# Kernel optimization log

Measured on AMD Instinct MI355X. Metric: run time of the kernel, lower is better.

The kernel has to match this reference:

```python
import jax, jax.numpy as jnp
import numpy as np

N_NODES = 50000
N_EDGES = 800000
IN_DIM = 128
HID = 64
HEADS = 4
EDGE_DIM = 3
NEG_SLOPE = 0.2  # PyG GATv2 default


def setup_inputs() -> dict:
    key = jax.random.key(0)
    ks = jax.random.split(key, 16)
    def glorot(k, shape):
        fan_in = shape[0]
        return (jax.random.normal(k, shape, jnp.float32) / jnp.sqrt(jnp.float32(fan_in)))
    x = jax.random.normal(ks[0], (N_NODES, IN_DIM), jnp.float32)
    edge_attr = jax.random.normal(ks[1], (N_EDGES, EDGE_DIM), jnp.float32)
    edge_index = jax.random.randint(ks[2], (2, N_EDGES), 0, N_NODES, jnp.int32)
    # layer 1: GATv2Conv(IN_DIM -> HID, heads=HEADS, edge_dim=3, concat=True)
    W1l = glorot(ks[3], (IN_DIM, HEADS * HID))
    W1r = glorot(ks[4], (IN_DIM, HEADS * HID))
    W1e = glorot(ks[5], (EDGE_DIM, HEADS * HID))
    att1 = glorot(ks[6], (HEADS, HID))
    b1 = jnp.zeros((HEADS * HID,), jnp.float32)
    # layer 2: GATv2Conv(HEADS*HID -> 1, heads=1, edge_dim=3, concat=False)
    W2l = glorot(ks[7], (HEADS * HID, 1))
    W2r = glorot(ks[8], (HEADS * HID, 1))
    W2e = glorot(ks[9], (EDGE_DIM, 1))
    att2 = glorot(ks[10], (1, 1))
    b2 = jnp.zeros((1,), jnp.float32)
    return {"x": x, "edge_attr": edge_attr, "W1l": W1l, "W1r": W1r, "W1e": W1e,
            "att1": att1, "b1": b1, "W2l": W2l, "W2r": W2r, "W2e": W2e,
            "att2": att2, "b2": b2, "edge_index": edge_index}


def _add_self_loops(edge_index, edge_attr, n_nodes):
    # PyG GATv2Conv add_self_loops=True with fill_value='mean' for edge_attr
    loops = jnp.arange(n_nodes, dtype=edge_index.dtype)
    ei = jnp.concatenate([edge_index, jnp.stack([loops, loops])], axis=1)
    loop_attr = jnp.broadcast_to(edge_attr.mean(axis=0, keepdims=True),
                                 (n_nodes, edge_attr.shape[1]))
    ea = jnp.concatenate([edge_attr, loop_attr], axis=0)
    return ei, ea


def _gatv2(x, edge_index, edge_attr, Wl, Wr, We, att, bias, heads, concat):
    n = x.shape[0]
    c = Wl.shape[1] // heads
    src, dst = edge_index[0], edge_index[1]
    xl = (x @ Wl).reshape(n, heads, c)   # source-side transform
    xr = (x @ Wr).reshape(n, heads, c)   # target-side transform
    ef = (edge_attr @ We).reshape(-1, heads, c)
    m = jax.nn.leaky_relu(xl[src] + xr[dst] + ef, NEG_SLOPE)   # [E,H,C]
    logits = jnp.einsum('ehc,hc->eh', m, att)                  # [E,H]
    mx = jax.ops.segment_max(logits, dst, num_segments=n)      # segment softmax over dst
    a = jnp.exp(logits - mx[dst])
    denom = jax.ops.segment_sum(a, dst, num_segments=n)
    alpha = a / denom[dst]                                     # [E,H]
    out = jax.ops.segment_sum(xl[src] * alpha[:, :, None], dst, num_segments=n)  # [N,H,C]
    out = out.reshape(n, heads * c) if concat else out.mean(axis=1)
    return out + bias


def reference(x, edge_attr, W1l, W1r, W1e, att1, b1, W2l, W2r, W2e, att2, b2, edge_index):
    n = x.shape[0]
    ei, ea = _add_self_loops(edge_index, edge_attr, n)
    h = _gatv2(x, ei, ea, W1l, W1r, W1e, att1, b1, HEADS, True)
    h = jax.nn.elu(h)  # dropout identity in eval mode
    gat_scores = _gatv2(h, ei, ea, W2l, W2r, W2e, att2, b2, 1, False).squeeze(-1)
    portfolio_weights = jax.nn.softmax(gat_scores, axis=0)
    return portfolio_weights, gat_scores
```

## Files before the change

kernel.cpp:

```cpp
#include <hip/hip_runtime.h>
#include <hip/hip_bf16.h>
#include <hip/hip_fp16.h>

typedef __attribute__((ext_vector_type(8))) short short8;
typedef __attribute__((ext_vector_type(4))) float floatx4;
typedef _Float16 h2 __attribute__((ext_vector_type(2)));
typedef _Float16 h4 __attribute__((ext_vector_type(4)));
typedef _Float16 h8 __attribute__((ext_vector_type(8)));
typedef __fp16 fp16x2 __attribute__((ext_vector_type(2)));

#define N_NODESC 50000
#define MPAD     50016
#define N_EDGESC 800000
#define E_TOTC   850000
#define IN_DIMC  128
#define FDIM     256
#define HEADSC   4
#define HIDC     64
#define NEG_SLOPE 0.2f
#define RESCALE_THR 8.0f

#define SCAN_TILE 1024
#define SCAN_NB   ((N_NODESC + SCAN_TILE - 1) / SCAN_TILE)

__device__ __forceinline__ float wave_sum(float v){
  #pragma unroll
  for (int m = 32; m > 0; m >>= 1) v += __shfl_xor(v, m, 64);
  return v;
}
__device__ __forceinline__ float wave_max(float v){
  #pragma unroll
  for (int m = 32; m > 0; m >>= 1) v = fmaxf(v, __shfl_xor(v, m, 64));
  return v;
}
__device__ __forceinline__ float g16_sum(float v){
  #pragma unroll
  for (int m = 8; m > 0; m >>= 1) v += __shfl_xor(v, m, 64);
  return v;
}
__device__ __forceinline__ float g16_max(float v){
  #pragma unroll
  for (int m = 8; m > 0; m >>= 1) v = fmaxf(v, __shfl_xor(v, m, 64));
  return v;
}

__device__ __forceinline__ h2 f2h2(float v){
  return __builtin_bit_cast(h2, __builtin_amdgcn_cvt_pkrtz(v, v));
}
__device__ __forceinline__ float fdot2(h2 a, h2 b, float c){
  return __builtin_amdgcn_fdot2(__builtin_bit_cast(fp16x2, a),
                                __builtin_bit_cast(fp16x2, b), c, false);
}

__global__ __launch_bounds__(256) void k_mean(const float* __restrict__ ea,
                                              float* __restrict__ meanacc){
  float s0 = 0.f, s1 = 0.f, s2 = 0.f;
  for (int i = blockIdx.x * blockDim.x + threadIdx.x; i < N_EDGESC;
       i += gridDim.x * blockDim.x){
    s0 += ea[i*3+0]; s1 += ea[i*3+1]; s2 += ea[i*3+2];
  }
  s0 = wave_sum(s0); s1 = wave_sum(s1); s2 = wave_sum(s2);
  __shared__ float red[3][4];
  int lane = threadIdx.x & 63, w = threadIdx.x >> 6;
  if (lane == 0){ red[0][w] = s0; red[1][w] = s1; red[2][w] = s2; }
  __syncthreads();
  if (threadIdx.x == 0){
    float t0 = 0.f, t1 = 0.f, t2 = 0.f;
    for (int i = 0; i < 4; i++){ t0 += red[0][i]; t1 += red[1][i]; t2 += red[2][i]; }
    atomicAdd(&meanacc[0], t0); atomicAdd(&meanacc[1], t1); atomicAdd(&meanacc[2], t2);
  }
}

__global__ __launch_bounds__(256) void k_count(const int* __restrict__ ei,
                                               int* __restrict__ deg){
  int e = blockIdx.x * blockDim.x + threadIdx.x;
  if (e >= N_EDGESC) return;
  atomicAdd(&deg[ei[N_EDGESC + e]], 1);
}

__global__ __launch_bounds__(256) void k_cvtx(const float* __restrict__ x,
                                              _Float16* __restrict__ xb){
  size_t tid = (size_t)blockIdx.x * 256 + threadIdx.x;
  size_t base = tid * 4;
  const size_t NELEM = (size_t)N_NODESC * IN_DIMC;
  h4 o;
  if (base + 3 < NELEM){
    const float4* xp = (const float4*)(x + base);
    float4 v = *xp;
    o[0] = (_Float16)v.x; o[1] = (_Float16)v.y;
    o[2] = (_Float16)v.z; o[3] = (_Float16)v.w;
  } else {
    #pragma unroll
    for (int f = 0; f < 4; f++){
      size_t i = base + f;
      float v = (i < NELEM) ? x[i] : 0.f;
      o[f] = (_Float16)v;
    }
  }
  *(h4*)(xb + base) = o;
}

__global__ __launch_bounds__(256) void k_cvtw(const float* __restrict__ W1l,
                                              const float* __restrict__ W1r,
                                              _Float16* __restrict__ Bfrag){
  int idx = blockIdx.x * 256 + threadIdx.x;
  int mat = idx >> 15;
  int r   = idx & 32767;
  int k   = r >> 8, n = r & 255;
  float v = mat ? W1r[r] : W1l[r];
  int pos = (mat << 15) + (((k >> 3) << 8) + n) * 8 + (k & 7);
  Bfrag[pos] = (_Float16)v;
}

__global__ __launch_bounds__(256) void k_gemm_mfma(const _Float16* __restrict__ xb,
                                                   const _Float16* __restrict__ Bfrag,
                                                   _Float16* __restrict__ xl,
                                                   _Float16* __restrict__ xr){
  const int mat = blockIdx.y;
  const int r0  = blockIdx.x * 32;
  const int w = threadIdx.x >> 6, lane = threadIdx.x & 63;
  const int quad = lane >> 4, l16 = lane & 15;
  const _Float16* Bm = Bfrag + ((size_t)mat << 15);
  _Float16* C = mat ? xr : xl;

  h8 afr[2][4];
  #pragma unroll
  for (int ms = 0; ms < 2; ms++)
    #pragma unroll
    for (int ks = 0; ks < 4; ks++){
      const _Float16* p = xb + (size_t)(r0 + ms*16 + l16) * IN_DIMC + ks*32 + quad*8;
      afr[ms][ks] = *reinterpret_cast<const h8*>(p);
    }
  const int n0 = w * 64;
  floatx4 acc[2][4];
  #pragma unroll
  for (int ms = 0; ms < 2; ms++)
    #pragma unroll
    for (int ns = 0; ns < 4; ns++){
      floatx4 z = {0.f, 0.f, 0.f, 0.f};
      acc[ms][ns] = z;
    }
  #pragma unroll
  for (int ks = 0; ks < 4; ks++){
    #pragma unroll
    for (int ns = 0; ns < 4; ns++){
      int n = n0 + ns*16 + l16;
      int kblk = ks*4 + quad;
      h8 bfr = *reinterpret_cast<const h8*>(Bm + ((size_t)kblk*256 + n)*8);
      acc[0][ns] = __builtin_amdgcn_mfma_f32_16x16x32_f16(afr[0][ks], bfr, acc[0][ns], 0, 0, 0);
      acc[1][ns] = __builtin_amdgcn_mfma_f32_16x16x32_f16(afr[1][ks], bfr, acc[1][ns], 0, 0, 0);
    }
  }
  #pragma unroll
  for (int ms = 0; ms < 2; ms++)
    #pragma unroll
    for (int ns = 0; ns < 4; ns++){
      int col = n0 + ns*16 + l16;
      #pragma unroll
      for (int rg = 0; rg < 4; rg++){
        int row = r0 + ms*16 + quad*4 + rg;
        C[(size_t)row * FDIM + col] = (_Float16)acc[ms][ns][rg];
      }
    }
}

__global__ __launch_bounds__(256) void k_scan_pa(const int* __restrict__ deg,
                                                 int* __restrict__ pre,
                                                 int* __restrict__ bsum){
  int b = blockIdx.x, t = threadIdx.x;
  int lane = t & 63, w = t >> 6;
  int base = b * SCAN_TILE + t * 4;
  int4 v = {0, 0, 0, 0};
  if (base + 3 < N_NODESC){
    v = *(const int4*)(deg + base);
    v.x += 1; v.y += 1; v.z += 1; v.w += 1;
  } else {
    if (base + 0 < N_NODESC) v.x = deg[base + 0] + 1;
    if (base + 1 < N_NODESC) v.y = deg[base + 1] + 1;
    if (base + 2 < N_NODESC) v.z = deg[base + 2] + 1;
    if (base + 3 < N_NODESC) v.w = deg[base + 3] + 1;
  }
  int s = v.x + v.y + v.z + v.w;
  int inc = s;
  #pragma unroll
  for (int off = 1; off < 64; off <<= 1){
    int u = __shfl_up(inc, off, 64);
    if (lane >= off) inc += u;
  }
  __shared__ int wsum[4];
  if (lane == 63) wsum[w] = inc;
  __syncthreads();
  int wadd = 0;
  #pragma unroll
  for (int i = 0; i < 4; i++) if (i < w) wadd += wsum[i];
  int excl = inc - s + wadd;
  if (base + 3 < N_NODESC){
    int4 o;
    o.x = excl; o.y = o.x + v.x; o.z = o.y + v.y; o.w = o.z + v.z;
    *(int4*)(pre + base) = o;
  } else {
    int run = excl;
    if (base + 0 < N_NODESC){ pre[base + 0] = run; run += v.x; }
    if (base + 1 < N_NODESC){ pre[base + 1] = run; run += v.y; }
    if (base + 2 < N_NODESC){ pre[base + 2] = run; run += v.z; }
    if (base + 3 < N_NODESC){ pre[base + 3] = run; }
  }
  if (t == 255) bsum[b] = wsum[0] + wsum[1] + wsum[2] + wsum[3];
}

__global__ __launch_bounds__(64) void k_scan_pb(const int* __restrict__ bsum,
                                                int* __restrict__ boff,
                                                int* __restrict__ offsets){
  int lane = threadIdx.x;
  int s = (lane < SCAN_NB) ? bsum[lane] : 0;
  int inc = s;
  #pragma unroll
  for (int off = 1; off < 64; off <<= 1){
    int u = __shfl_up(inc, off, 64);
    if (lane >= off) inc += u;
  }
  if (lane < SCAN_NB) boff[lane] = inc - s;
  if (lane == 63) offsets[N_NODESC] = inc;
}

__global__ __launch_bounds__(256) void k_scan_pc(const int* __restrict__ pre,
                                                 const int* __restrict__ boff,
                                                 int* __restrict__ offsets,
                                                 int* __restrict__ cursor){
  int b = blockIdx.x;
  int base = b * SCAN_TILE + threadIdx.x * 4;
  int add = boff[b];
  if (base + 3 < N_NODESC){
    int4 p = *(const int4*)(pre + base);
    p.x += add; p.y += add; p.z += add; p.w += add;
    *(int4*)(offsets + base) = p;
    *(int4*)(cursor + base) = p;
  } else {
    #pragma unroll
    for (int f = 0; f < 4; f++){
      int i = base + f;
      if (i < N_NODESC){ int vv = pre[i] + add; offsets[i] = vv; cursor[i] = vv; }
    }
  }
}

__global__ __launch_bounds__(256) void k_scatter(const int* __restrict__ ei,
                                                 const float* __restrict__ ea,
                                                 const float* __restrict__ meanacc,
                                                 const int* __restrict__ offsets,
                                                 int* __restrict__ cursor,
                                                 float4* __restrict__ rec){
  int e = blockIdx.x * blockDim.x + threadIdx.x;
  if (e >= E_TOTC) return;
  int pos; float4 r;
  if (e < N_EDGESC){
    int src = ei[e], dst = ei[N_EDGESC + e];
    r.x = __int_as_float(src);
    r.y = ea[e*3+0]; r.z = ea[e*3+1]; r.w = ea[e*3+2];
    pos = atomicAdd(&cursor[dst], 1);
  } else {
    int i = e - N_EDGESC;
    const float inv = 1.0f / (float)N_EDGESC;
    r.x = __int_as_float(i);
    r.y = meanacc[0]*inv; r.z = meanacc[1]*inv; r.w = meanacc[2]*inv;
    pos = offsets[i + 1] - 1;
  }
  rec[pos] = r;
}

__global__ __launch_bounds__(256, 4) void k_attn1(const int* __restrict__ offsets,
                                                  const float4* __restrict__ rec,
                                                  const _Float16* __restrict__ xl,
                                                  const _Float16* __restrict__ xr,
                                                  const float* __restrict__ W1e,
                                                  const float* __restrict__ att1,
                                                  const float* __restrict__ b1,
                                                  const float* __restrict__ W2l,
                                                  const float* __restrict__ W2r,
                                                  float* __restrict__ sl,
                                                  float* __restrict__ sr){
  const int t = threadIdx.x, lane = t & 63, w = t >> 6;
  const int n = blockIdx.x * 4 + w;
  const int half = lane >> 5, l32 = lane & 31;
  const int f0 = l32 * 8;

  h2 xrp[4], w0p[4], w1p[4], w2p[4], atp[4];
  {
    h8 xw = *(const h8*)(xr + (size_t)n * FDIM + f0);
    #pragma unroll
    for (int k = 0; k < 4; k++) xrp[k] = h2{xw[2*k], xw[2*k+1]};
    float4 a0 = *(const float4*)(W1e + f0);
    float4 a1 = *(const float4*)(W1e + f0 + 4);
    w0p[0]=h2{(_Float16)a0.x,(_Float16)a0.y}; w0p[1]=h2{(_Float16)a0.z,(_Float16)a0.w};
    w0p[2]=h2{(_Float16)a1.x,(_Float16)a1.y}; w0p[3]=h2{(_Float16)a1.z,(_Float16)a1.w};
    float4 b0 = *(const float4*)(W1e + FDIM + f0);
    float4 b4 = *(const float4*)(W1e + FDIM + f0 + 4);
    w1p[0]=h2{(_Float16)b0.x,(_Float16)b0.y}; w1p[1]=h2{(_Float16)b0.z,(_Float16)b0.w};
    w1p[2]=h2{(_Float16)b4.x,(_Float16)b4.y}; w1p[3]=h2{(_Float16)b4.z,(_Float16)b4.w};
    float4 c0 = *(const float4*)(W1e + 2*FDIM + f0);
    float4 c4 = *(const float4*)(W1e + 2*FDIM + f0 + 4);
    w2p[0]=h2{(_Float16)c0.x,(_Float16)c0.y}; w2p[1]=h2{(_Float16)c0.z,(_Float16)c0.w};
    w2p[2]=h2{(_Float16)c4.x,(_Float16)c4.y}; w2p[3]=h2{(_Float16)c4.z,(_Float16)c4.w};
    float4 d0 = *(const float4*)(att1 + f0);
    float4 d4 = *(const float4*)(att1 + f0 + 4);
    atp[0]=h2{(_Float16)d0.x,(_Float16)d0.y}; atp[1]=h2{(_Float16)d0.z,(_Float16)d0.w};
    atp[2]=h2{(_Float16)d4.x,(_Float16)d4.y}; atp[3]=h2{(_Float16)d4.z,(_Float16)d4.w};
  }
  const h2 nsl2 = h2{(_Float16)NEG_SLOPE, (_Float16)NEG_SLOPE};
  const int beg = offsets[n], end = offsets[n + 1];
  const int last = end - 1;

  float m = -1e30f, den = 0.f;
  float acc[8] = {0.f,0.f,0.f,0.f,0.f,0.f,0.f,0.f};

  int j = beg + half;
  float4 rc  = rec[min(j, last)];
  float4 rcn = rec[min(j + 2, last)];
  unsigned off0 = ((unsigned)__float_as_int(rc.x) << 8) + f0;
  h8 raw = *(const h8*)(xl + off0);

  for (; j < end; j += 2){
    unsigned offn = ((unsigned)__float_as_int(rcn.x) << 8) + f0;
    h8 rawn = *(const h8*)(xl + offn);
    const float e0 = rc.y, e1 = rc.z, e2 = rc.w;
    rc = rcn;
    rcn = rec[min(j + 4, last)];

    h2 he0 = f2h2(e0), he1 = f2h2(e1), he2 = f2h2(e2);
    float pp = 0.f;
    #pragma unroll
    for (int k = 0; k < 4; k++){
      h2 xk = h2{raw[2*k], raw[2*k+1]};
      h2 v = xk + xrp[k] + he0*w0p[k] + he1*w1p[k] + he2*w2p[k];
      v = __builtin_elementwise_max(v, nsl2 * v);
      pp = fdot2(v, atp[k], pp);
    }
    pp += __shfl_xor(pp, 1, 64);
    pp += __shfl_xor(pp, 2, 64);
    pp += __shfl_xor(pp, 4, 64);

    if (pp > m + RESCALE_THR){
      float corr = __expf(m - pp);
      den *= corr;
      #pragma unroll
      for (int k = 0; k < 8; k++) acc[k] *= corr;
      m = pp;
    }
    float al = __expf(pp - m);
    den += al;
    #pragma unroll
    for (int k = 0; k < 8; k++) acc[k] = fmaf((float)raw[k], al, acc[k]);

    raw = rawn;
  }

  float m_o   = __shfl_xor(m, 32, 64);
  float den_o = __shfl_xor(den, 32, 64);
  float m_t = fmaxf(m, m_o);
  float sc   = __expf(m - m_t);
  float sc_o = __expf(m_o - m_t);
  float den_t = den * sc + den_o * sc_o;
  float invd = 1.0f / den_t;

  float4 bb0 = *(const float4*)(b1 + f0);
  float4 bb4 = *(const float4*)(b1 + f0 + 4);
  float bb[8] = {bb0.x,bb0.y,bb0.z,bb0.w,bb4.x,bb4.y,bb4.z,bb4.w};
  float hv[8];
  #pragma unroll
  for (int k = 0; k < 8; k++){
    float a_o = __shfl_xor(acc[k], 32, 64);
    float tot = acc[k] * sc + a_o * sc_o;
    float h = tot * invd + bb[k];
    hv[k] = (h > 0.f) ? h : (__expf(h) - 1.f);
  }
  float4 l0 = *(const float4*)(W2l + f0);
  float4 l4 = *(const float4*)(W2l + f0 + 4);
  float4 r0 = *(const float4*)(W2r + f0);
  float4 r4 = *(const float4*)(W2r + f0 + 4);
  float wl[8] = {l0.x,l0.y,l0.z,l0.w,l4.x,l4.y,l4.z,l4.w};
  float wr[8] = {r0.x,r0.y,r0.z,r0.w,r4.x,r4.y,r4.z,r4.w};
  float pa = 0.f, pb = 0.f;
  #pragma unroll
  for (int k = 0; k < 8; k++){ pa += hv[k]*wl[k]; pb += hv[k]*wr[k]; }
  #pragma unroll
  for (int msk = 16; msk > 0; msk >>= 1){
    pa += __shfl_xor(pa, msk, 64);
    pb += __shfl_xor(pb, msk, 64);
  }
  if (lane == 0){ sl[n] = pa; sr[n] = pb; }
}

__device__ __forceinline__ unsigned fkey(float f){
  unsigned u = __float_as_uint(f);
  return u ^ ((u >> 31) ? 0xFFFFFFFFu : 0x80000000u);
}
__device__ __forceinline__ float funkey(unsigned k){
  unsigned u = (k >> 31) ? (k ^ 0x80000000u) : ~k;
  return __uint_as_float(u);
}

__global__ __launch_bounds__(256) void k_attn2(const int* __restrict__ offsets,
                                               const float4* __restrict__ rec,
                                               const float* __restrict__ W2e,
                                               const float* __restrict__ att2,
                                               const float* __restrict__ b2p,
                                               const float* __restrict__ sl,
                                               const float* __restrict__ sr,
                                               float* __restrict__ scores,
                                               float* __restrict__ out){
  int t = threadIdx.x, l16 = t & 15;
  int n = blockIdx.x * 16 + (t >> 4);
  if (n >= N_NODESC) return;
  const float attv = att2[0];
  const float w2e0 = W2e[0], w2e1 = W2e[1], w2e2 = W2e[2];
  const float srn = sr[n];
  int beg = offsets[n], end = offsets[n + 1];
  float m = -1e30f, den = 0.f, num = 0.f;
  for (int j = beg + l16; j < end; j += 16){
    float4 rc = rec[j];
    float slv = sl[__float_as_int(rc.x)];
    float v = slv + srn + rc.y*w2e0 + rc.z*w2e1 + rc.w*w2e2;
    v = (v > 0.f) ? v : NEG_SLOPE * v;
    float lg = v * attv;
    float mn = fmaxf(m, lg);
    float corr = __expf(m - mn);
    float pe   = __expf(lg - mn);
    den = den * corr + pe;
    num = num * corr + pe * slv;
    m = mn;
  }
  float mg = g16_max(m);
  float scale = __expf(m - mg);
  float deng = g16_sum(den * scale);
  float numg = g16_sum(num * scale);
  if (l16 == 0){
    float s = numg / deng + b2p[0];
    scores[n] = s;
    out[N_NODESC + n] = s;
  }
}

__global__ __launch_bounds__(256) void k_smax_max(const float* __restrict__ scores,
                                                  unsigned* __restrict__ redmax){
  float m = -1e30f;
  for (int i = blockIdx.x * blockDim.x + threadIdx.x; i < N_NODESC;
       i += gridDim.x * blockDim.x)
    m = fmaxf(m, scores[i]);
  m = wave_max(m);
  __shared__ float ws_[4];
  int lane = threadIdx.x & 63, w = threadIdx.x >> 6;
  if (lane == 0) ws_[w] = m;
  __syncthreads();
  if (threadIdx.x == 0){
    for (int i = 1; i < 4; i++) m = fmaxf(m, ws_[i]);
    atomicMax(redmax, fkey(m));
  }
}

__global__ __launch_bounds__(256) void k_smax_sum(const float* __restrict__ scores,
                                                  const unsigned* __restrict__ redmax,
                                                  float* __restrict__ redsum){
  float mx = funkey(*redmax);
  float s = 0.f;
  for (int i = blockIdx.x * blockDim.x + threadIdx.x; i < N_NODESC;
       i += gridDim.x * blockDim.x)
    s += __expf(scores[i] - mx);
  s = wave_sum(s);
  __shared__ float ws_[4];
  int lane = threadIdx.x & 63, w = threadIdx.x >> 6;
  if (lane == 0) ws_[w] = s;
  __syncthreads();
  if (threadIdx.x == 0){
    float t = 0.f;
    for (int i = 0; i < 4; i++) t += ws_[i];
    atomicAdd(redsum, t);
  }
}

__global__ __launch_bounds__(256) void k_smax_write(const float* __restrict__ scores,
                                                    const unsigned* __restrict__ redmax,
                                                    const float* __restrict__ redsum,
                                                    float* __restrict__ out){
  int i = blockIdx.x * blockDim.x + threadIdx.x;
  if (i >= N_NODESC) return;
  float mx = funkey(*redmax);
  float inv = 1.0f / (*redsum);
  out[i] = __expf(scores[i] - mx) * inv;
}

extern "C" void kernel_launch(void* const* d_in, const int* in_sizes, int n_in,
                              void* d_out, int out_size, void* d_ws, size_t ws_size,
                              hipStream_t stream) {
  const float* x    = (const float*)d_in[0];
  const float* ea   = (const float*)d_in[1];
  const float* W1l  = (const float*)d_in[2];
  const float* W1r  = (const float*)d_in[3];
  const float* W1e  = (const float*)d_in[4];
  const float* att1 = (const float*)d_in[5];
  const float* b1   = (const float*)d_in[6];
  const float* W2l  = (const float*)d_in[7];
  const float* W2r  = (const float*)d_in[8];
  const float* W2e  = (const float*)d_in[9];
  const float* att2 = (const float*)d_in[10];
  const float* b2   = (const float*)d_in[11];
  const int*   ei   = (const int*)d_in[12];
  float* out = (float*)d_out;

  char* w = (char*)d_ws;
  size_t off = 0;
  auto alloc = [&](size_t bytes) -> char* {
    char* p = w + off;
    off = (off + bytes + 255) & ~(size_t)255;
    return p;
  };
  float*    meanacc = (float*)alloc(16);
  unsigned* redmax  = (unsigned*)alloc(8);
  float*    redsum  = (float*)((char*)redmax + 4);
  int*      deg     = (int*)alloc((size_t)N_NODESC * 4);
  size_t zero_bytes = off;
  int*   offsets = (int*)alloc((size_t)(N_NODESC + 1) * 4);
  int*   cursor  = (int*)alloc((size_t)N_NODESC * 4);
  int*   pre     = (int*)alloc((size_t)N_NODESC * 4);
  int*   bsum    = (int*)alloc((size_t)SCAN_NB * 4);
  int*   boff    = (int*)alloc((size_t)SCAN_NB * 4);
  float4* rec    = (float4*)alloc((size_t)E_TOTC * 16);
  float* sl      = (float*)alloc((size_t)N_NODESC * 4);
  float* sr      = (float*)alloc((size_t)N_NODESC * 4);
  float* scores  = (float*)alloc((size_t)N_NODESC * 4);
  _Float16* xb    = (_Float16*)alloc((size_t)MPAD * IN_DIMC * 2);
  _Float16* Bfrag = (_Float16*)alloc((size_t)2 * 128 * 256 * 2);
  _Float16* xl    = (_Float16*)alloc((size_t)MPAD * FDIM * 2);
  _Float16* xr    = (_Float16*)alloc((size_t)MPAD * FDIM * 2);
  (void)ws_size; (void)in_sizes; (void)n_in; (void)out_size;

  hipMemsetAsync(d_ws, 0, zero_bytes, stream);

  k_mean  <<<400, 256, 0, stream>>>(ea, meanacc);
  k_count <<<(N_EDGESC + 255) / 256, 256, 0, stream>>>(ei, deg);
  k_cvtx  <<<(int)(((size_t)MPAD * IN_DIMC / 4 + 255) / 256), 256, 0, stream>>>(x, xb);
  k_cvtw  <<<256, 256, 0, stream>>>(W1l, W1r, Bfrag);
  k_scan_pa<<<SCAN_NB, 256, 0, stream>>>(deg, pre, bsum);
  k_scan_pb<<<1, 64, 0, stream>>>(bsum, boff, offsets);
  k_scan_pc<<<SCAN_NB, 256, 0, stream>>>(pre, boff, offsets, cursor);
  k_scatter<<<(E_TOTC + 255) / 256, 256, 0, stream>>>(ei, ea, meanacc, offsets,
                                                      cursor, rec);
  {
    dim3 g(MPAD / 32, 2);
    k_gemm_mfma<<<g, 256, 0, stream>>>(xb, Bfrag, xl, xr);
  }
  k_attn1 <<<N_NODESC / 4, 256, 0, stream>>>(offsets, rec, xl, xr,
                                             W1e, att1, b1, W2l, W2r, sl, sr);
  k_attn2 <<<(N_NODESC + 15) / 16, 256, 0, stream>>>(offsets, rec, W2e, att2, b2,
                                                     sl, sr, scores, out);
  k_smax_max <<<256, 256, 0, stream>>>(scores, redmax);
  k_smax_sum <<<256, 256, 0, stream>>>(scores, redmax, redsum);
  k_smax_write<<<(N_NODESC + 255) / 256, 256, 0, stream>>>(scores, redmax, redsum, out);
}
```

Measured before the change: 335.6 us.

## Precompute edge ranks during counting and process 4 edges per wave in attention

The degree-count kernel now stores each edge's atomic rank, so the scatter computes positions as offset plus rank and no longer needs a second round of atomics on a cursor array. The layer-1 attention kernel is restructured so that each wave handles four edges at once, using 16 lanes of 16 features each instead of two halves of 32 lanes with 8 features. This gives more memory-level parallelism per gather, at the cost of more registers and an extra reduction stage for merging the online softmax. The change also adds a 3.2MB rank buffer that has to be written and read back.

```diff
diff --git a/kernel.cpp b/kernel.cpp
--- a/kernel.cpp
+++ b/kernel.cpp
@@ -72,10 +72,11 @@
 }
 
 __global__ __launch_bounds__(256) void k_count(const int* __restrict__ ei,
-                                               int* __restrict__ deg){
+                                               int* __restrict__ deg,
+                                               int* __restrict__ rank){
   int e = blockIdx.x * blockDim.x + threadIdx.x;
   if (e >= N_EDGESC) return;
-  atomicAdd(&deg[ei[N_EDGESC + e]], 1);
+  rank[e] = atomicAdd(&deg[ei[N_EDGESC + e]], 1);
 }
 
 __global__ __launch_bounds__(256) void k_cvtx(const float* __restrict__ x,
@@ -225,8 +226,7 @@
 
 __global__ __launch_bounds__(256) void k_scan_pc(const int* __restrict__ pre,
                                                  const int* __restrict__ boff,
-                                                 int* __restrict__ offsets,
-                                                 int* __restrict__ cursor){
+                                                 int* __restrict__ offsets){
   int b = blockIdx.x;
   int base = b * SCAN_TILE + threadIdx.x * 4;
   int add = boff[b];
@@ -234,12 +234,11 @@
     int4 p = *(const int4*)(pre + base);
     p.x += add; p.y += add; p.z += add; p.w += add;
     *(int4*)(offsets + base) = p;
-    *(int4*)(cursor + base) = p;
   } else {
     #pragma unroll
     for (int f = 0; f < 4; f++){
       int i = base + f;
-      if (i < N_NODESC){ int vv = pre[i] + add; offsets[i] = vv; cursor[i] = vv; }
+      if (i < N_NODESC) offsets[i] = pre[i] + add;
     }
   }
 }
@@ -248,7 +247,7 @@
                                                  const float* __restrict__ ea,
                                                  const float* __restrict__ meanacc,
                                                  const int* __restrict__ offsets,
-                                                 int* __restrict__ cursor,
+                                                 const int* __restrict__ rank,
                                                  float4* __restrict__ rec){
   int e = blockIdx.x * blockDim.x + threadIdx.x;
   if (e >= E_TOTC) return;
@@ -257,7 +256,7 @@
     int src = ei[e], dst = ei[N_EDGESC + e];
     r.x = __int_as_float(src);
     r.y = ea[e*3+0]; r.z = ea[e*3+1]; r.w = ea[e*3+2];
-    pos = atomicAdd(&cursor[dst], 1);
+    pos = offsets[dst] + rank[e];
   } else {
     int i = e - N_EDGESC;
     const float inv = 1.0f / (float)N_EDGESC;
@@ -281,109 +280,125 @@
                                                   float* __restrict__ sr){
   const int t = threadIdx.x, lane = t & 63, w = t >> 6;
   const int n = blockIdx.x * 4 + w;
-  const int half = lane >> 5, l32 = lane & 31;
-  const int f0 = l32 * 8;
-
-  h2 xrp[4], w0p[4], w1p[4], w2p[4], atp[4];
+  const int q = lane >> 4, l16 = lane & 15;
+  const int f0 = l16 * 16;
+
+  h2 xrp[8], w0p[8], w1p[8], w2p[8], atp[8];
   {
-    h8 xw = *(const h8*)(xr + (size_t)n * FDIM + f0);
-    #pragma unroll
-    for (int k = 0; k < 4; k++) xrp[k] = h2{xw[2*k], xw[2*k+1]};
-    float4 a0 = *(const float4*)(W1e + f0);
-    float4 a1 = *(const float4*)(W1e + f0 + 4);
-    w0p[0]=h2{(_Float16)a0.x,(_Float16)a0.y}; w0p[1]=h2{(_Float16)a0.z,(_Float16)a0.w};
-    w0p[2]=h2{(_Float16)a1.x,(_Float16)a1.y}; w0p[3]=h2{(_Float16)a1.z,(_Float16)a1.w};
-    float4 b0 = *(const float4*)(W1e + FDIM + f0);
-    float4 b4 = *(const float4*)(W1e + FDIM + f0 + 4);
-    w1p[0]=h2{(_Float16)b0.x,(_Float16)b0.y}; w1p[1]=h2{(_Float16)b0.z,(_Float16)b0.w};
-    w1p[2]=h2{(_Float16)b4.x,(_Float16)b4.y}; w1p[3]=h2{(_Float16)b4.z,(_Float16)b4.w};
-    float4 c0 = *(const float4*)(W1e + 2*FDIM + f0);
-    float4 c4 = *(const float4*)(W1e + 2*FDIM + f0 + 4);
-    w2p[0]=h2{(_Float16)c0.x,(_Float16)c0.y}; w2p[1]=h2{(_Float16)c0.z,(_Float16)c0.w};
-    w2p[2]=h2{(_Float16)c4.x,(_Float16)c4.y}; w2p[3]=h2{(_Float16)c4.z,(_Float16)c4.w};
-    float4 d0 = *(const float4*)(att1 + f0);
-    float4 d4 = *(const float4*)(att1 + f0 + 4);
-    atp[0]=h2{(_Float16)d0.x,(_Float16)d0.y}; atp[1]=h2{(_Float16)d0.z,(_Float16)d0.w};
-    atp[2]=h2{(_Float16)d4.x,(_Float16)d4.y}; atp[3]=h2{(_Float16)d4.z,(_Float16)d4.w};
+    h8 xw0 = *(const h8*)(xr + (size_t)n * FDIM + f0);
+    h8 xw1 = *(const h8*)(xr + (size_t)n * FDIM + f0 + 8);
+    #pragma unroll
+    for (int k = 0; k < 4; k++){
+      xrp[k]   = h2{xw0[2*k], xw0[2*k+1]};
+      xrp[4+k] = h2{xw1[2*k], xw1[2*k+1]};
+    }
+    #pragma unroll
+    for (int g = 0; g < 4; g++){
+      float4 a = *(const float4*)(W1e + f0 + 4*g);
+      w0p[2*g]   = h2{(_Float16)a.x, (_Float16)a.y};
+      w0p[2*g+1] = h2{(_Float16)a.z, (_Float16)a.w};
+      float4 b = *(const float4*)(W1e + FDIM + f0 + 4*g);
+      w1p[2*g]   = h2{(_Float16)b.x, (_Float16)b.y};
+      w1p[2*g+1] = h2{(_Float16)b.z, (_Float16)b.w};
+      float4 c = *(const float4*)(W1e + 2*FDIM + f0 + 4*g);
+      w2p[2*g]   = h2{(_Float16)c.x, (_Float16)c.y};
+      w2p[2*g+1] = h2{(_Float16)c.z, (_Float16)c.w};
+      float4 d = *(const float4*)(att1 + f0 + 4*g);
+      atp[2*g]   = h2{(_Float16)d.x, (_Float16)d.y};
+      atp[2*g+1] = h2{(_Float16)d.z, (_Float16)d.w};
+    }
   }
   const h2 nsl2 = h2{(_Float16)NEG_SLOPE, (_Float16)NEG_SLOPE};
   const int beg = offsets[n], end = offsets[n + 1];
   const int last = end - 1;
 
   float m = -1e30f, den = 0.f;
-  float acc[8] = {0.f,0.f,0.f,0.f,0.f,0.f,0.f,0.f};
-
-  int j = beg + half;
+  float acc[16];
+  #pragma unroll
+  for (int k = 0; k < 16; k++) acc[k] = 0.f;
+
+  int j = beg + q;
   float4 rc  = rec[min(j, last)];
-  float4 rcn = rec[min(j + 2, last)];
-  unsigned off0 = ((unsigned)__float_as_int(rc.x) << 8) + f0;
-  h8 raw = *(const h8*)(xl + off0);
-
-  for (; j < end; j += 2){
-    unsigned offn = ((unsigned)__float_as_int(rcn.x) << 8) + f0;
-    h8 rawn = *(const h8*)(xl + offn);
+  float4 rcn = rec[min(j + 4, last)];
+  unsigned b0 = ((unsigned)__float_as_int(rc.x) << 8) + f0;
+  h8 rawA = *(const h8*)(xl + b0);
+  h8 rawB = *(const h8*)(xl + b0 + 8);
+
+  for (; j < end; j += 4){
+    unsigned bn = ((unsigned)__float_as_int(rcn.x) << 8) + f0;
+    h8 rawAn = *(const h8*)(xl + bn);
+    h8 rawBn = *(const h8*)(xl + bn + 8);
     const float e0 = rc.y, e1 = rc.z, e2 = rc.w;
     rc = rcn;
-    rcn = rec[min(j + 4, last)];
+    rcn = rec[min(j + 8, last)];
 
     h2 he0 = f2h2(e0), he1 = f2h2(e1), he2 = f2h2(e2);
     float pp = 0.f;
     #pragma unroll
     for (int k = 0; k < 4; k++){
-      h2 xk = h2{raw[2*k], raw[2*k+1]};
-      h2 v = xk + xrp[k] + he0*w0p[k] + he1*w1p[k] + he2*w2p[k];
+      h2 v = h2{rawA[2*k], rawA[2*k+1]} + xrp[k]
+           + he0*w0p[k] + he1*w1p[k] + he2*w2p[k];
       v = __builtin_elementwise_max(v, nsl2 * v);
       pp = fdot2(v, atp[k], pp);
     }
+    #pragma unroll
+    for (int k = 0; k < 4; k++){
+      h2 v = h2{rawB[2*k], rawB[2*k+1]} + xrp[4+k]
+           + he0*w0p[4+k] + he1*w1p[4+k] + he2*w2p[4+k];
+      v = __builtin_elementwise_max(v, nsl2 * v);
+      pp = fdot2(v, atp[4+k], pp);
+    }
     pp += __shfl_xor(pp, 1, 64);
     pp += __shfl_xor(pp, 2, 64);
-    pp += __shfl_xor(pp, 4, 64);
 
     if (pp > m + RESCALE_THR){
       float corr = __expf(m - pp);
       den *= corr;
       #pragma unroll
-      for (int k = 0; k < 8; k++) acc[k] *= corr;
+      for (int k = 0; k < 16; k++) acc[k] *= corr;
       m = pp;
     }
     float al = __expf(pp - m);
     den += al;
     #pragma unroll
-    for (int k = 0; k < 8; k++) acc[k] = fmaf((float)raw[k], al, acc[k]);
-
-    raw = rawn;
-  }
-
-  float m_o   = __shfl_xor(m, 32, 64);
-  float den_o = __shfl_xor(den, 32, 64);
-  float m_t = fmaxf(m, m_o);
-  float sc   = __expf(m - m_t);
-  float sc_o = __expf(m_o - m_t);
-  float den_t = den * sc + den_o * sc_o;
-  float invd = 1.0f / den_t;
-
-  float4 bb0 = *(const float4*)(b1 + f0);
-  float4 bb4 = *(const float4*)(b1 + f0 + 4);
-  float bb[8] = {bb0.x,bb0.y,bb0.z,bb0.w,bb4.x,bb4.y,bb4.z,bb4.w};
-  float hv[8];
-  #pragma unroll
-  for (int k = 0; k < 8; k++){
-    float a_o = __shfl_xor(acc[k], 32, 64);
-    float tot = acc[k] * sc + a_o * sc_o;
-    float h = tot * invd + bb[k];
-    hv[k] = (h > 0.f) ? h : (__expf(h) - 1.f);
-  }
-  float4 l0 = *(const float4*)(W2l + f0);
-  float4 l4 = *(const float4*)(W2l + f0 + 4);
-  float4 r0 = *(const float4*)(W2r + f0);
-  float4 r4 = *(const float4*)(W2r + f0 + 4);
-  float wl[8] = {l0.x,l0.y,l0.z,l0.w,l4.x,l4.y,l4.z,l4.w};
-  float wr[8] = {r0.x,r0.y,r0.z,r0.w,r4.x,r4.y,r4.z,r4.w};
+    for (int k = 0; k < 8; k++) acc[k]     = fmaf((float)rawA[k], al, acc[k]);
+    #pragma unroll
+    for (int k = 0; k < 8; k++) acc[8 + k] = fmaf((float)rawB[k], al, acc[8 + k]);
+
+    rawA = rawAn; rawB = rawBn;
+  }
+
+  #pragma unroll
+  for (int st = 0; st < 2; st++){
+    const int msk = 16 << st;
+    float m_o   = __shfl_xor(m, msk, 64);
+    float den_o = __shfl_xor(den, msk, 64);
+    float m_t = fmaxf(m, m_o);
+    float sA = __expf(m - m_t), sB = __expf(m_o - m_t);
+    den = den * sA + den_o * sB;
+    #pragma unroll
+    for (int k = 0; k < 16; k++){
+      float a_o = __shfl_xor(acc[k], msk, 64);
+      acc[k] = acc[k] * sA + a_o * sB;
+    }
+    m = m_t;
+  }
+  float invd = 1.0f / den;
+
   float pa = 0.f, pb = 0.f;
   #pragma unroll
-  for (int k = 0; k < 8; k++){ pa += hv[k]*wl[k]; pb += hv[k]*wr[k]; }
-  #pragma unroll
-  for (int msk = 16; msk > 0; msk >>= 1){
+  for (int g = 0; g < 4; g++){
+    float4 bb = *(const float4*)(b1 + f0 + 4*g);
+    float4 wl = *(const float4*)(W2l + f0 + 4*g);
+    float4 wr = *(const float4*)(W2r + f0 + 4*g);
+    float h;
+    h = acc[4*g+0]*invd + bb.x; h = (h>0.f)?h:(__expf(h)-1.f); pa += h*wl.x; pb += h*wr.x;
+    h = acc[4*g+1]*invd + bb.y; h = (h>0.f)?h:(__expf(h)-1.f); pa += h*wl.y; pb += h*wr.y;
+    h = acc[4*g+2]*invd + bb.z; h = (h>0.f)?h:(__expf(h)-1.f); pa += h*wl.z; pb += h*wr.z;
+    h = acc[4*g+3]*invd + bb.w; h = (h>0.f)?h:(__expf(h)-1.f); pa += h*wl.w; pb += h*wr.w;
+  }
+  #pragma unroll
+  for (int msk = 8; msk > 0; msk >>= 1){
     pa += __shfl_xor(pa, msk, 64);
     pb += __shfl_xor(pb, msk, 64);
   }
@@ -519,7 +534,7 @@
   int*      deg     = (int*)alloc((size_t)N_NODESC * 4);
   size_t zero_bytes = off;
   int*   offsets = (int*)alloc((size_t)(N_NODESC + 1) * 4);
-  int*   cursor  = (int*)alloc((size_t)N_NODESC * 4);
+  int*   rank    = (int*)alloc((size_t)N_EDGESC * 4);
   int*   pre     = (int*)alloc((size_t)N_NODESC * 4);
   int*   bsum    = (int*)alloc((size_t)SCAN_NB * 4);
   int*   boff    = (int*)alloc((size_t)SCAN_NB * 4);
@@ -536,14 +551,14 @@
   hipMemsetAsync(d_ws, 0, zero_bytes, stream);
 
   k_mean  <<<400, 256, 0, stream>>>(ea, meanacc);
-  k_count <<<(N_EDGESC + 255) / 256, 256, 0, stream>>>(ei, deg);
+  k_count <<<(N_EDGESC + 255) / 256, 256, 0, stream>>>(ei, deg, rank);
   k_cvtx  <<<(int)(((size_t)MPAD * IN_DIMC / 4 + 255) / 256), 256, 0, stream>>>(x, xb);
   k_cvtw  <<<256, 256, 0, stream>>>(W1l, W1r, Bfrag);
   k_scan_pa<<<SCAN_NB, 256, 0, stream>>>(deg, pre, bsum);
   k_scan_pb<<<1, 64, 0, stream>>>(bsum, boff, offsets);
-  k_scan_pc<<<SCAN_NB, 256, 0, stream>>>(pre, boff, offsets, cursor);
+  k_scan_pc<<<SCAN_NB, 256, 0, stream>>>(pre, boff, offsets);
   k_scatter<<<(E_TOTC + 255) / 256, 256, 0, stream>>>(ei, ea, meanacc, offsets,
-                                                      cursor, rec);
+                                                      rank, rec);
   {
     dim3 g(MPAD / 32, 2);
     k_gemm_mfma<<<g, 256, 0, stream>>>(xb, Bfrag, xl, xr);
```

Result: slower. 343.8 us (+2.4%).
